# Kernel optimization log

Measured on AMD Instinct MI355X. Metric: run time of the kernel, lower is better.

## Reference

```python
import jax, jax.numpy as jnp
import numpy as np

B = 32
N_PER = 4096
N = B * N_PER
E = 2_097_152
D_IN = 32
D_OUT = 32
NUM_G_RELS = 14
NUM_ATTN_RELS = 10


def setup_inputs() -> dict:
    key = jax.random.key(0)
    ks = jax.random.split(key, 12)
    feat = jax.random.normal(ks[0], (N, D_IN), jnp.float32)
    src = jax.random.randint(ks[1], (E,), 0, N)
    dst = jax.random.randint(ks[2], (E,), 0, N)
    etype = jax.random.randint(ks[3], (E,), 0, NUM_ATTN_RELS)
    norm = jax.random.uniform(ks[4], (E,), jnp.float32)
    index1 = jax.random.randint(ks[5], (N,), 0, 2)  # path-node mask
    # first NUM_G_RELS nodes of each subgraph carry distinct relation slots -> unique scatter indices
    index2 = jnp.tile((jnp.arange(N_PER) < NUM_G_RELS).astype(jnp.int32), B)
    f2 = jnp.tile(jnp.arange(N_PER) % NUM_G_RELS, B).astype(jnp.int32)
    tar_rel = jnp.tile((jnp.arange(N_PER) == 0).astype(jnp.int32), B)  # one target node per graph
    s = 0.1
    W_w = jax.random.normal(ks[6], (D_IN, D_OUT), jnp.float32) * s
    b_w = jnp.zeros((D_OUT,), jnp.float32)
    W2 = jax.random.normal(ks[7], (3 * D_OUT, D_OUT), jnp.float32) * s
    b2 = jnp.zeros((D_OUT,), jnp.float32)
    attn_rel_emb = jax.random.normal(ks[8], (NUM_ATTN_RELS, D_OUT), jnp.float32) * s
    self_loop_w = jax.random.normal(ks[9], (D_IN, D_OUT), jnp.float32) * s
    W_line = jax.random.normal(ks[10], (D_OUT, D_OUT), jnp.float32) * s
    b_line = jnp.zeros((D_OUT,), jnp.float32)
    zero_path = jax.random.normal(ks[11], (1, D_OUT), jnp.float32) * s
    return {"feat": feat, "norm": norm, "W_w": W_w, "b_w": b_w, "W2": W2, "b2": b2,
            "attn_rel_emb": attn_rel_emb, "self_loop_w": self_loop_w, "W_line": W_line,
            "b_line": b_line, "zero_path": zero_path, "src": src, "dst": dst, "etype": etype,
            "index1": index1, "index2": index2, "f2": f2, "tar_rel": tar_rel,
            "n_per": N_PER, "num_g_rels": NUM_G_RELS}


def reference(feat, norm, W_w, b_w, W2, b2, attn_rel_emb, self_loop_w, W_line, b_line,
              zero_path, src, dst, etype, index1, index2, f2, tar_rel, n_per, num_g_rels):
    n_nodes, _ = feat.shape
    D = W_w.shape[1]
    # --- edge-wise relation-gated MLP (msg_func) ---
    et = attn_rel_emb[etype]                       # [E, D]
    w1 = feat[src] @ W_w + b_w                     # [E, D]
    cat = jnp.concatenate([et + w1, et - w1, et * w1], axis=1)  # [E, 3D]
    msg = (cat @ W2 + b2) * norm[:, None]          # [E, D] (edge weight w == 1)
    # --- SumAggregator: sum of msgs (alpha = ones) + self-loop term ---
    h = jax.ops.segment_sum(msg, dst, num_segments=n_nodes) + feat @ self_loop_w
    nf = jax.nn.relu(h @ W_line + b_line)          # cg_node_feats [N, D]
    # --- per-subgraph relation scatter + path attention (vectorized over batch) ---
    Bn = n_nodes // n_per
    nf_b = nf.reshape(Bn, n_per, D)
    mask2 = index2.reshape(Bn, n_per) != 0
    f2b = f2.reshape(Bn, n_per) + 1                # index_offset = 1
    write_idx = jnp.where(mask2, f2b, num_g_rels + 1)  # route masked rows to dump slot

    def scatter_one(idx, feats):
        buf = jnp.zeros((num_g_rels + 2, D), nf.dtype).at[idx].set(feats)
        return buf[:num_g_rels + 1]

    batch_rel_emds = jax.vmap(scatter_one)(write_idx, nf_b)  # [B, num_g_rels+1, D]
    tar1 = (tar_rel.reshape(Bn, n_per) == 1).astype(nf.dtype)
    target_rel_emd = jnp.einsum('bn,bnd->bd', tar1, nf_b)    # [B, D] (one-hot select)
    p1 = index1.reshape(Bn, n_per) == 1
    scores = jnp.where(p1, jnp.einsum('bnd,bd->bn', nf_b, target_rel_emd), -1e30)
    alpha = jax.nn.softmax(scores, axis=1)                   # segmented softmax over path nodes
    agg = jnp.einsum('bn,bnd->bd', alpha, nf_b)
    path_agg_emd = jnp.where(p1.any(axis=1)[:, None], agg, zero_path)  # [B, D]
    return batch_rel_emds, target_rel_emd, path_agg_emd
```

## Files before the change

kernel.cpp:

```cpp
#include <hip/hip_runtime.h>


#define N_PER_C 4096
#define NGR 14
#define NAR 10
#define NZB 68
#define KSP 8
#define BKN 128
#define NBMAX 1024
#define TSC 4096
#define CHK 2048

typedef unsigned short u16;
typedef unsigned int u32;
typedef _Float16 hv2 __attribute__((ext_vector_type(2)));
union U32H2 { u32 u; hv2 h; };

__device__ __forceinline__ float b2f(u16 u) {
    union { u32 i; float f; } x; x.i = ((u32)u) << 16; return x.f;
}
__device__ __forceinline__ u16 f2bf(float f) {
    union { float f; u32 i; } x; x.f = f;
    u32 r = x.i + 0x7fff + ((x.i >> 16) & 1);
    return (u16)(r >> 16);
}
__device__ __forceinline__ float LD(const void* p, size_t i, int isf32) {
    return isf32 ? ((const float*)p)[i] : b2f(((const u16*)p)[i]);
}
__device__ __forceinline__ void ST_OUT(void* p, size_t i, float v, int isf32) {
    if (isf32) ((float*)p)[i] = v;
    else ((u16*)p)[i] = f2bf(v);
}
__device__ __forceinline__ u32 pkh(float a, float b) {
    U32H2 c; c.h = (hv2){(_Float16)a, (_Float16)b}; return c.u;
}
__device__ __forceinline__ hv2 ash2(u32 w) { U32H2 c; c.u = w; return c.h; }

__device__ __forceinline__ int probe_flag(const u32* featw) {
    int cnt = 0;
#pragma unroll
    for (int i = 0; i < 256; i += 64) {
        u32 w = featw[i + (threadIdx.x & 63)];
        u32 lo = w & 0xffffu;
        u32 e = (lo >> 7) & 0xffu;
        cnt += ((e >= 100 && e <= 140) || lo == 0) ? 1 : 0;
    }
    unsigned long long m = __ballot(cnt >= 3);
    return (__popcll(m) < 32) ? 1 : 0;
}

__global__ __launch_bounds__(256) void k_prep(
        const u32* __restrict__ featw,
        const void* W_w, const void* b_w, const void* W2, const void* b2v,
        const void* attn, const void* slw, const void* W_line, const void* b_line,
        u32* __restrict__ outw, int out_size,
        float* Wwf, float* bwf, float* Af, float* slwf, float* Wlf, float* blf,
        float* Cf, float* ctf, u32* at2, u32* bcnt, int NB, int* flag) {
    int t = threadIdx.x;
    int b = blockIdx.x;
    int isf32 = probe_flag(featw);
    if (b < NZB) {
        int words = isf32 ? out_size : out_size / 2;
        for (int i = b * 256 + t; i < words; i += NZB * 256) outw[i] = 0;
        for (int i = b * 256 + t; i < NB; i += NZB * 256) bcnt[i] = 0u;
        return;
    }
    if (t == 0) flag[0] = isf32;
    for (int i = t; i < 1024; i += 256) {
        int k = i >> 5, c = i & 31;
        Wwf[i]  = LD(W_w, i, isf32);
        slwf[i] = LD(slw, i, isf32);
        Wlf[i]  = LD(W_line, i, isf32);
        Af[i]   = LD(W2, k * 32 + c, isf32) - LD(W2, (32 + k) * 32 + c, isf32);
        Cf[i]   = LD(W2, (64 + k) * 32 + c, isf32);
    }
    for (int i = t; i < NAR * 16; i += 256) {
        int tt = i >> 4, q = i & 15;
        at2[i] = pkh(LD(attn, tt * 32 + 2 * q, isf32),
                     LD(attn, tt * 32 + 2 * q + 1, isf32));
    }
    for (int i = t; i < NAR * 32; i += 256) {
        int tt = i >> 5, j = i & 31;
        float s = LD(b2v, j, isf32);
        for (int k = 0; k < 32; ++k) {
            float a = LD(attn, tt * 32 + k, isf32);
            s += a * (LD(W2, k * 32 + j, isf32) + LD(W2, (32 + k) * 32 + j, isf32));
        }
        ctf[i] = s;
    }
    if (t < 32) { bwf[t] = LD(b_w, t, isf32); blf[t] = LD(b_line, t, isf32); }
}

__global__ __launch_bounds__(256) void k1_node(const void* __restrict__ feat,
                        const float* __restrict__ Wwf,
                        const float* __restrict__ bwf, const float* __restrict__ slwf,
                        u32* __restrict__ gbuf, u32* __restrict__ h, int N,
                        const int* __restrict__ dst, u32* __restrict__ bcnt,
                        int E, int NB, const int* __restrict__ flag) {
    __shared__ u32 lh[NBMAX];
    int tid = threadIdx.x;
    int gid = blockIdx.x * 256 + tid;
    int isf32 = flag[0];
    for (int i = tid; i < NB; i += 256) lh[i] = 0u;
    __syncthreads();
    if (gid < N) {
        int n = gid;
        float f[32];
        if (isf32) {
            const float4* fr = (const float4*)((const float*)feat + (size_t)n * 32);
#pragma unroll
            for (int q = 0; q < 8; ++q) {
                float4 v = fr[q];
                f[q * 4 + 0] = v.x; f[q * 4 + 1] = v.y; f[q * 4 + 2] = v.z; f[q * 4 + 3] = v.w;
            }
        } else {
            const uint4* fr = (const uint4*)((const u16*)feat + (size_t)n * 32);
#pragma unroll
            for (int q = 0; q < 4; ++q) {
                uint4 v = fr[q];
                u32 ww[4] = {v.x, v.y, v.z, v.w};
#pragma unroll
                for (int r = 0; r < 4; ++r) {
                    f[q * 8 + 2 * r]     = b2f((u16)(ww[r] & 0xffff));
                    f[q * 8 + 2 * r + 1] = b2f((u16)(ww[r] >> 16));
                }
            }
        }
        float g[32], hh[32];
#pragma unroll
        for (int j = 0; j < 32; ++j) { g[j] = bwf[j]; hh[j] = 0.f; }
#pragma unroll
        for (int k = 0; k < 32; ++k) {
            float fk = f[k];
#pragma unroll
            for (int j = 0; j < 32; ++j) {
                g[j]  += fk * Wwf[k * 32 + j];
                hh[j] += fk * slwf[k * 32 + j];
            }
        }
        u32* go = gbuf + (size_t)n * 16;
#pragma unroll
        for (int q = 0; q < 16; ++q) go[q] = pkh(g[2 * q], g[2 * q + 1]);
        u32* ho = h + (size_t)n * 16;
#pragma unroll
        for (int q = 0; q < 16; ++q) ho[q] = pkh(hh[2 * q], hh[2 * q + 1]);
    }
    int EB = (E + gridDim.x - 1) / gridDim.x;
    int e0 = blockIdx.x * EB;
    int e1 = e0 + EB; if (e1 > E) e1 = E;
    for (int e = e0 + tid; e < e1; e += 256)
        atomicAdd(&lh[((u32)dst[e]) / BKN], 1u);
    __syncthreads();
    for (int i = tid; i < NB; i += 256) {
        u32 c = lh[i];
        if (c) atomicAdd(&bcnt[i], c);
    }
}

__global__ __launch_bounds__(256) void kB_scan(const u32* __restrict__ bcnt,
                                               u32* __restrict__ bbase,
                                               u32* __restrict__ bcur, int NB) {
    __shared__ u32 red[256];
    int tid = threadIdx.x;
    u32 c4[4]; u32 s = 0;
#pragma unroll
    for (int k = 0; k < 4; ++k) {
        int idx = tid * 4 + k;
        c4[k] = (idx < NB) ? bcnt[idx] : 0u;
        s += c4[k];
    }
    red[tid] = s;
    __syncthreads();
    for (int off = 1; off < 256; off <<= 1) {
        u32 v = (tid >= off) ? red[tid - off] : 0u;
        __syncthreads();
        red[tid] += v;
        __syncthreads();
    }
    u32 ex = red[tid] - s;
#pragma unroll
    for (int k = 0; k < 4; ++k) {
        int idx = tid * 4 + k;
        if (idx < NB) { bbase[idx] = ex; bcur[idx] = ex; ex += c4[k]; }
    }
    if (tid == 255) bbase[NB] = red[255];
}

__global__ __launch_bounds__(256) void kB_scatter(const int* __restrict__ src,
        const int* __restrict__ dst, const int* __restrict__ et,
        const void* __restrict__ norm, u32* __restrict__ bcur,
        uint2* __restrict__ pay, int E, int NB, const int* __restrict__ flag) {
    __shared__ u32 lcnt[NBMAX], loffA[NBMAX], loffB[NBMAX], lbase[NBMAX];
    __shared__ u32 red[256];
    __shared__ uint2 lbuf[TSC];
    __shared__ u16 lbkt[TSC];
    int tid = threadIdx.x;
    int base_e = blockIdx.x * TSC;
    int nval = E - base_e; if (nval > TSC) nval = TSC; if (nval < 0) nval = 0;
    int isf32 = flag[0];
    for (int i = tid; i < NB; i += 256) lcnt[i] = 0u;
    __syncthreads();
    u32 pk0[16], nw[16]; int bk[16];
#pragma unroll
    for (int i = 0; i < 16; ++i) {
        int e = base_e + i * 256 + tid;
        if (e < E) {
            int s = src[e], d = dst[e], t = et[e];
            float nr = LD(norm, e, isf32);
            pk0[i] = (u32)s | ((u32)t << 17) | ((u32)(d & (BKN - 1)) << 21);
            nw[i] = __float_as_uint(nr);
            bk[i] = ((u32)d) / BKN;
            atomicAdd(&lcnt[bk[i]], 1u);
        } else bk[i] = -1;
    }
    __syncthreads();
    u32 c4[4]; u32 s = 0;
#pragma unroll
    for (int k = 0; k < 4; ++k) {
        int idx = tid * 4 + k;
        c4[k] = (idx < NB) ? lcnt[idx] : 0u;
        s += c4[k];
    }
    red[tid] = s;
    __syncthreads();
    for (int off = 1; off < 256; off <<= 1) {
        u32 v = (tid >= off) ? red[tid - off] : 0u;
        __syncthreads();
        red[tid] += v;
        __syncthreads();
    }
    u32 ex = red[tid] - s;
#pragma unroll
    for (int k = 0; k < 4; ++k) {
        int idx = tid * 4 + k;
        if (idx < NB) { loffA[idx] = ex; loffB[idx] = ex; ex += c4[k]; }
    }
    __syncthreads();
    for (int b = tid; b < NB; b += 256) {
        u32 c = lcnt[b];
        if (c) lbase[b] = atomicAdd(&bcur[b], c);
    }
    __syncthreads();
#pragma unroll
    for (int i = 0; i < 16; ++i) {
        if (bk[i] >= 0) {
            u32 slot = atomicAdd(&loffB[bk[i]], 1u);
            lbuf[slot] = make_uint2(pk0[i], nw[i]);
            lbkt[slot] = (u16)bk[i];
        }
    }
    __syncthreads();
    for (int s2 = tid; s2 < nval; s2 += 256) {
        int b = lbkt[s2];
        u32 gpos = lbase[b] + (u32)s2 - loffA[b];
        pay[gpos] = lbuf[s2];
    }
}

__global__ __launch_bounds__(128) void kC_bucket(const u32* __restrict__ gbuf,
        const uint2* __restrict__ pay, const u32* __restrict__ bbase,
        const float* __restrict__ Af, const float* __restrict__ Cf,
        const float* __restrict__ ctf, const u32* __restrict__ at2,
        u32* __restrict__ h) {
    __shared__ uint2 lbuf[CHK];
    __shared__ u32 cnt_s[BKN];
    __shared__ u32 off_s[BKN];
    __shared__ u32 cur_s[BKN];
    __shared__ u32 scn_s[BKN];
    __shared__ u32 atl[16 * NAR];
    int tid = threadIdx.x;
    int b = blockIdx.x;
    for (int i = tid; i < 16 * NAR; i += 128) {
        int t = i >> 4, q = i & 15;
        atl[q * NAR + t] = at2[i];
    }
    int e0 = (int)bbase[b], e1 = (int)bbase[b + 1];

    float yg[32], x[32], nt[NAR];
#pragma unroll
    for (int j = 0; j < 32; ++j) { yg[j] = 0.f; x[j] = 0.f; }
#pragma unroll
    for (int t = 0; t < NAR; ++t) nt[t] = 0.f;

    for (int cb = e0; cb < e1; cb += CHK) {
        int nrec = e1 - cb; if (nrec > CHK) nrec = CHK;
        cnt_s[tid] = 0u;
        __syncthreads();
        for (int i = tid; i < nrec; i += 128)
            atomicAdd(&cnt_s[(pay[cb + i].x >> 21) & (BKN - 1)], 1u);
        __syncthreads();
        u32 myv = cnt_s[tid];
        scn_s[tid] = myv;
        __syncthreads();
        for (int s = 1; s < BKN; s <<= 1) {
            u32 v = (tid >= s) ? scn_s[tid - s] : 0u;
            __syncthreads();
            scn_s[tid] += v;
            __syncthreads();
        }
        u32 myoff = scn_s[tid] - myv;
        off_s[tid] = myoff;
        cur_s[tid] = myoff;
        __syncthreads();
        for (int i = tid; i < nrec; i += 128) {
            uint2 r = pay[cb + i];
            u32 d = (r.x >> 21) & (BKN - 1);
            u32 slot = atomicAdd(&cur_s[d], 1u);
            lbuf[slot] = r;
        }
        __syncthreads();
        {
            u32 myc = myv;
            uint2 rec = make_uint2(0u, 0u);
            uint4 GA = {0,0,0,0}, GB = {0,0,0,0}, GC = {0,0,0,0}, GD = {0,0,0,0};
            if (myc) {
                rec = lbuf[myoff];
                const uint4* g4 = (const uint4*)(gbuf + (size_t)(rec.x & 0x1FFFFu) * 16);
                GA = g4[0]; GB = g4[1]; GC = g4[2]; GD = g4[3];
            }
            for (u32 r = 0; r < myc; ++r) {
                uint2 rn = make_uint2(0u, 0u);
                uint4 HA = {0,0,0,0}, HB = {0,0,0,0}, HC = {0,0,0,0}, HD = {0,0,0,0};
                if (r + 1 < myc) {
                    rn = lbuf[myoff + r + 1];
                    const uint4* g4 = (const uint4*)(gbuf + (size_t)(rn.x & 0x1FFFFu) * 16);
                    HA = g4[0]; HB = g4[1]; HC = g4[2]; HD = g4[3];
                }
                int t = (int)((rec.x >> 17) & 0xFu);
                float nr = __uint_as_float(rec.y);
                u32 gw[16] = {GA.x, GA.y, GA.z, GA.w, GB.x, GB.y, GB.z, GB.w,
                              GC.x, GC.y, GC.z, GC.w, GD.x, GD.y, GD.z, GD.w};
#pragma unroll
                for (int q = 0; q < 16; ++q) {
                    hv2 gv = ash2(gw[q]);
                    hv2 av = ash2(atl[q * NAR + t]);
                    float ng0 = nr * (float)gv[0];
                    float ng1 = nr * (float)gv[1];
                    yg[2 * q]     += ng0;
                    yg[2 * q + 1] += ng1;
                    x[2 * q]      += ng0 * (float)av[0];
                    x[2 * q + 1]  += ng1 * (float)av[1];
                }
#pragma unroll
                for (int t2 = 0; t2 < NAR; ++t2) nt[t2] += (t2 == t) ? nr : 0.f;
                rec = rn;
                GA = HA; GB = HB; GC = HC; GD = HD;
            }
        }
        __syncthreads();
    }

    int n = b * BKN + tid;
    float o[32];
    const uint4* hr4 = (const uint4*)(h + (size_t)n * 16);
    uint4 v0 = hr4[0], v1 = hr4[1], v2 = hr4[2], v3 = hr4[3];
    u32 ww[16] = {v0.x, v0.y, v0.z, v0.w, v1.x, v1.y, v1.z, v1.w,
                  v2.x, v2.y, v2.z, v2.w, v3.x, v3.y, v3.z, v3.w};
#pragma unroll
    for (int r = 0; r < 16; ++r) {
        hv2 xh = ash2(ww[r]);
        o[2 * r]     = (float)xh[0];
        o[2 * r + 1] = (float)xh[1];
    }
#pragma unroll
    for (int t = 0; t < NAR; ++t) {
        float w = nt[t];
#pragma unroll
        for (int j = 0; j < 32; ++j) o[j] += w * ctf[t * 32 + j];
    }
#pragma unroll
    for (int k = 0; k < 32; ++k) {
        float a = yg[k], c = x[k];
#pragma unroll
        for (int j = 0; j < 32; ++j)
            o[j] += a * Af[k * 32 + j] + c * Cf[k * 32 + j];
    }
    u32* ho = h + (size_t)n * 16;
#pragma unroll
    for (int q = 0; q < 16; ++q) ho[q] = pkh(o[2 * q], o[2 * q + 1]);
}

__global__ __launch_bounds__(256) void k34_fused(const u32* __restrict__ h,
        const float* __restrict__ Wlf, const float* __restrict__ blf,
        const int* __restrict__ index2, const int* __restrict__ f2,
        const int* __restrict__ index1,
        void* __restrict__ out, size_t off_tar,
        float* __restrict__ part_m, float* __restrict__ part_l,
        float* __restrict__ part_a, const int* __restrict__ flag) {
    int blk = blockIdx.x;
    int b = blk / KSP, c = blk % KSP;
    int tid = threadIdx.x;
    int isf32 = flag[0];
    __shared__ float tg[32];
    __shared__ float red_m[256], red_l[256];
    __shared__ float red_a[256][33];

    if (tid < 32) {
        const u32* h0 = h + (size_t)b * N_PER_C * 16;
        float o = blf[tid];
#pragma unroll
        for (int k = 0; k < 32; ++k) {
            hv2 x = ash2(h0[k >> 1]);
            o += (float)x[k & 1] * Wlf[k * 32 + tid];
        }
        o = fmaxf(o, 0.f);
        tg[tid] = o;
        if (c == 0) ST_OUT(out, off_tar + (size_t)b * 32 + tid, o, isf32);
    }
    __syncthreads();
    float tv[32];
#pragma unroll
    for (int j = 0; j < 32; ++j) tv[j] = tg[j];

    float m = -1e30f, l = 0.f, a[32];
#pragma unroll
    for (int j = 0; j < 32; ++j) a[j] = 0.f;

    const int R = N_PER_C / KSP;
    for (int rr = 0; rr < R / 256; ++rr) {
        int n = b * N_PER_C + c * R + rr * 256 + tid;
        float hr[32];
        const uint4* h4 = (const uint4*)(h + (size_t)n * 16);
#pragma unroll
        for (int q = 0; q < 4; ++q) {
            uint4 v = h4[q];
            u32 ww[4] = {v.x, v.y, v.z, v.w};
#pragma unroll
            for (int r2 = 0; r2 < 4; ++r2) {
                hv2 x = ash2(ww[r2]);
                hr[q * 8 + 2 * r2]     = (float)x[0];
                hr[q * 8 + 2 * r2 + 1] = (float)x[1];
            }
        }
        float o[32];
#pragma unroll
        for (int j = 0; j < 32; ++j) o[j] = blf[j];
#pragma unroll
        for (int k = 0; k < 32; ++k) {
            float hk = hr[k];
#pragma unroll
            for (int j = 0; j < 32; ++j) o[j] += hk * Wlf[k * 32 + j];
        }
#pragma unroll
        for (int j = 0; j < 32; ++j) o[j] = fmaxf(o[j], 0.f);
        if (index2[n] != 0) {
            int idx = f2[n] + 1;
            if (idx >= 0 && idx <= NGR) {
                size_t bse = ((size_t)(b * (NGR + 1) + idx)) * 32;
#pragma unroll
                for (int j = 0; j < 32; ++j) ST_OUT(out, bse + j, o[j], isf32);
            }
        }
        if (index1[n] == 1) {
            float dot = 0.f;
#pragma unroll
            for (int j = 0; j < 32; ++j) dot += o[j] * tv[j];
            if (dot > m) {
                float cc = __expf(m - dot);
                l *= cc;
#pragma unroll
                for (int j = 0; j < 32; ++j) a[j] *= cc;
                m = dot;
            }
            float w = __expf(dot - m);
            l += w;
#pragma unroll
            for (int j = 0; j < 32; ++j) a[j] += w * o[j];
        }
    }
    red_m[tid] = m; red_l[tid] = l;
#pragma unroll
    for (int j = 0; j < 32; ++j) red_a[tid][j] = a[j];
    __syncthreads();
    for (int s = 128; s >= 1; s >>= 1) {
        if (tid < s) {
            float m1 = red_m[tid], m2 = red_m[tid + s];
            float M = fmaxf(m1, m2);
            float c1 = __expf(m1 - M), c2 = __expf(m2 - M);
            red_l[tid] = red_l[tid] * c1 + red_l[tid + s] * c2;
#pragma unroll
            for (int j = 0; j < 32; ++j)
                red_a[tid][j] = red_a[tid][j] * c1 + red_a[tid + s][j] * c2;
            red_m[tid] = M;
        }
        __syncthreads();
    }
    if (tid == 0) { part_m[blk] = red_m[0]; part_l[blk] = red_l[0]; }
    if (tid < 32) part_a[(size_t)blk * 32 + tid] = red_a[0][tid];
}

__global__ __launch_bounds__(64) void k4b_merge(const float* __restrict__ part_m,
                                                const float* __restrict__ part_l,
                                                const float* __restrict__ part_a,
                                                const void* __restrict__ zero_path,
                                                void* __restrict__ out,
                                                size_t off_path,
                                                const int* __restrict__ flag) {
    int b = blockIdx.x;
    int j = threadIdx.x;
    int isf32 = flag[0];
    if (j >= 32) return;
    float M = -1e30f;
#pragma unroll
    for (int i = 0; i < KSP; ++i) M = fmaxf(M, part_m[b * KSP + i]);
    float L = 0.f, A = 0.f;
#pragma unroll
    for (int i = 0; i < KSP; ++i) {
        float c = __expf(part_m[b * KSP + i] - M);
        L += part_l[b * KSP + i] * c;
        A += part_a[(size_t)(b * KSP + i) * 32 + j] * c;
    }
    float o = (L > 0.f) ? (A / L) : LD(zero_path, j, isf32);
    ST_OUT(out, off_path + (size_t)b * 32 + j, o, isf32);
}

extern "C" void kernel_launch(void* const* d_in, const int* in_sizes, int n_in,
                              void* d_out, int out_size, void* d_ws, size_t ws_size,
                              hipStream_t stream) {
    const void* feat     = d_in[0];
    const void* norm     = d_in[1];
    const void* W_w      = d_in[2];
    const void* b_w      = d_in[3];
    const void* W2       = d_in[4];
    const void* b2v      = d_in[5];
    const void* attn     = d_in[6];
    const void* slw      = d_in[7];
    const void* W_line   = d_in[8];
    const void* b_line   = d_in[9];
    const void* zeroPath = d_in[10];
    const int* src       = (const int*)d_in[11];
    const int* dst       = (const int*)d_in[12];
    const int* etype     = (const int*)d_in[13];
    const int* index1    = (const int*)d_in[14];
    const int* index2    = (const int*)d_in[15];
    const int* f2        = (const int*)d_in[16];

    int N  = in_sizes[0] / 32;
    int E  = in_sizes[1];
    int Bn = N / N_PER_C;
    int NB = N / BKN;

    char* base  = (char*)d_ws;
    int* flag   = (int*)base;
    float* Wwf  = (float*)(base + 64);
    float* bwf  = Wwf + 1024;
    float* Af   = bwf + 32;
    float* slwf = Af + 1024;
    float* Wlf  = slwf + 1024;
    float* blf  = Wlf + 1024;
    float* Cf   = blf + 32;
    float* ctf  = Cf + 1024;
    u32*  at2   = (u32*)(ctf + NAR * 32);
    float* part_m = (float*)(at2 + NAR * 16);
    float* part_l = part_m + (size_t)Bn * KSP;
    float* part_a = part_l + (size_t)Bn * KSP;
    char* pa = (char*)(part_a + (size_t)Bn * KSP * 32);
    pa = (char*)(((size_t)pa + 255) & ~(size_t)255);
    u32* bcnt  = (u32*)pa;
    u32* bbase = bcnt + NBMAX;
    u32* bcur  = bbase + NBMAX + 1;
    char* pb = (char*)(bcur + NBMAX);
    pb = (char*)(((size_t)pb + 255) & ~(size_t)255);
    uint2* pay  = (uint2*)pb;
    u32* gbuf   = (u32*)(pay + (size_t)E);
    u32* h      = gbuf + (size_t)N * 16;

    size_t off_tar  = (size_t)Bn * (NGR + 1) * 32;
    size_t off_path = off_tar + (size_t)Bn * 32;

    k_prep<<<NZB + 1, 256, 0, stream>>>((const u32*)feat,
                                        W_w, b_w, W2, b2v, attn, slw, W_line, b_line,
                                        (u32*)d_out, out_size,
                                        Wwf, bwf, Af, slwf, Wlf, blf,
                                        Cf, ctf, at2, bcnt, NB, flag);
    k1_node<<<(N + 255) / 256, 256, 0, stream>>>(feat, Wwf, bwf, slwf, gbuf, h, N,
                                                 dst, bcnt, E, NB, flag);
    kB_scan<<<1, 256, 0, stream>>>(bcnt, bbase, bcur, NB);
    kB_scatter<<<(E + TSC - 1) / TSC, 256, 0, stream>>>(src, dst, etype, norm,
                                                        bcur, pay, E, NB, flag);
    kC_bucket<<<NB, 128, 0, stream>>>(gbuf, pay, bbase, Af, Cf, ctf, at2, h);
    k34_fused<<<Bn * KSP, 256, 0, stream>>>(h, Wlf, blf, index2, f2, index1,
                                            d_out, off_tar,
                                            part_m, part_l, part_a, flag);
    k4b_merge<<<Bn, 64, 0, stream>>>(part_m, part_l, part_a, zeroPath,
                                     d_out, off_path, flag);
}
```

Before: 280.8 us.

## Split each destination node's edge accumulation across two threads in bucket kernel

The bucket aggregation kernel now runs 256 threads per block, with two lanes per destination node, each accumulating half of the 32 feature dimensions. The gather prefetch depth goes from one to two edges ahead, and the per-relation attention table is pre-converted to float2 in shared memory. The halves are combined with a lane shuffle, and only the even lane does the final projection and write. Chunk size also rises to 2560. This aims to raise memory-level parallelism and occupancy for the random gathers, at the cost of idle odd lanes in the epilogue and more shared memory.

```diff
diff --git a/kernel.cpp b/kernel.cpp
--- a/kernel.cpp
+++ b/kernel.cpp
@@ -9,7 +9,7 @@
 #define BKN 128
 #define NBMAX 1024
 #define TSC 4096
-#define CHK 2048
+#define CHK 2560
 
 typedef unsigned short u16;
 typedef unsigned int u32;
@@ -257,52 +257,54 @@
     }
 }
 
-__global__ __launch_bounds__(128) void kC_bucket(const u32* __restrict__ gbuf,
+__global__ __launch_bounds__(256) void kC_bucket(const u32* __restrict__ gbuf,
         const uint2* __restrict__ pay, const u32* __restrict__ bbase,
         const float* __restrict__ Af, const float* __restrict__ Cf,
         const float* __restrict__ ctf, const u32* __restrict__ at2,
         u32* __restrict__ h) {
     __shared__ uint2 lbuf[CHK];
-    __shared__ u32 cnt_s[BKN];
-    __shared__ u32 off_s[BKN];
-    __shared__ u32 cur_s[BKN];
-    __shared__ u32 scn_s[BKN];
-    __shared__ u32 atl[16 * NAR];
+    __shared__ u32 cnt_s[BKN], off_s[BKN], cur_s[BKN], scn_s[BKN];
+    __shared__ float2 atf[16 * NAR];
     int tid = threadIdx.x;
     int b = blockIdx.x;
-    for (int i = tid; i < 16 * NAR; i += 128) {
+    int lane = tid & 63;
+    int w = tid >> 6;
+    int nodeloc = w * 32 + (lane >> 1);
+    int hf = lane & 1;
+    int hbase = hf * 8;
+    for (int i = tid; i < 16 * NAR; i += 256) {
         int t = i >> 4, q = i & 15;
-        atl[q * NAR + t] = at2[i];
+        hv2 p = ash2(at2[i]);
+        atf[q * NAR + t] = make_float2((float)p[0], (float)p[1]);
     }
     int e0 = (int)bbase[b], e1 = (int)bbase[b + 1];
 
-    float yg[32], x[32], nt[NAR];
-#pragma unroll
-    for (int j = 0; j < 32; ++j) { yg[j] = 0.f; x[j] = 0.f; }
+    float yg[16], x[16], nt[NAR];
+#pragma unroll
+    for (int j = 0; j < 16; ++j) { yg[j] = 0.f; x[j] = 0.f; }
 #pragma unroll
     for (int t = 0; t < NAR; ++t) nt[t] = 0.f;
 
     for (int cb = e0; cb < e1; cb += CHK) {
         int nrec = e1 - cb; if (nrec > CHK) nrec = CHK;
-        cnt_s[tid] = 0u;
-        __syncthreads();
-        for (int i = tid; i < nrec; i += 128)
+        if (tid < BKN) cnt_s[tid] = 0u;
+        __syncthreads();
+        for (int i = tid; i < nrec; i += 256)
             atomicAdd(&cnt_s[(pay[cb + i].x >> 21) & (BKN - 1)], 1u);
         __syncthreads();
-        u32 myv = cnt_s[tid];
-        scn_s[tid] = myv;
+        u32 cv = 0;
+        if (tid < BKN) { cv = cnt_s[tid]; scn_s[tid] = cv; }
         __syncthreads();
         for (int s = 1; s < BKN; s <<= 1) {
-            u32 v = (tid >= s) ? scn_s[tid - s] : 0u;
+            u32 v = 0;
+            if (tid < BKN && tid >= s) v = scn_s[tid - s];
             __syncthreads();
-            scn_s[tid] += v;
+            if (tid < BKN) scn_s[tid] += v;
             __syncthreads();
         }
-        u32 myoff = scn_s[tid] - myv;
-        off_s[tid] = myoff;
-        cur_s[tid] = myoff;
-        __syncthreads();
-        for (int i = tid; i < nrec; i += 128) {
+        if (tid < BKN) { u32 o = scn_s[tid] - cv; off_s[tid] = o; cur_s[tid] = o; }
+        __syncthreads();
+        for (int i = tid; i < nrec; i += 256) {
             uint2 r = pay[cb + i];
             u32 d = (r.x >> 21) & (BKN - 1);
             u32 slot = atomicAdd(&cur_s[d], 1u);
@@ -310,74 +312,92 @@
         }
         __syncthreads();
         {
-            u32 myc = myv;
-            uint2 rec = make_uint2(0u, 0u);
-            uint4 GA = {0,0,0,0}, GB = {0,0,0,0}, GC = {0,0,0,0}, GD = {0,0,0,0};
-            if (myc) {
-                rec = lbuf[myoff];
-                const uint4* g4 = (const uint4*)(gbuf + (size_t)(rec.x & 0x1FFFFu) * 16);
-                GA = g4[0]; GB = g4[1]; GC = g4[2]; GD = g4[3];
+            u32 myc = cnt_s[nodeloc];
+            u32 myoff = off_s[nodeloc];
+            uint2 r0 = make_uint2(0u, 0u), r1 = make_uint2(0u, 0u);
+            uint4 A0 = make_uint4(0,0,0,0), B0 = make_uint4(0,0,0,0);
+            uint4 A1 = make_uint4(0,0,0,0), B1 = make_uint4(0,0,0,0);
+            if (myc > 0) {
+                r0 = lbuf[myoff];
+                const uint4* g4 = (const uint4*)(gbuf + (size_t)(r0.x & 0x1FFFFu) * 16 + hbase);
+                A0 = g4[0]; B0 = g4[1];
+            }
+            if (myc > 1) {
+                r1 = lbuf[myoff + 1];
+                const uint4* g4 = (const uint4*)(gbuf + (size_t)(r1.x & 0x1FFFFu) * 16 + hbase);
+                A1 = g4[0]; B1 = g4[1];
             }
             for (u32 r = 0; r < myc; ++r) {
                 uint2 rn = make_uint2(0u, 0u);
-                uint4 HA = {0,0,0,0}, HB = {0,0,0,0}, HC = {0,0,0,0}, HD = {0,0,0,0};
-                if (r + 1 < myc) {
-                    rn = lbuf[myoff + r + 1];
-                    const uint4* g4 = (const uint4*)(gbuf + (size_t)(rn.x & 0x1FFFFu) * 16);
-                    HA = g4[0]; HB = g4[1]; HC = g4[2]; HD = g4[3];
+                uint4 An = make_uint4(0,0,0,0), Bn = make_uint4(0,0,0,0);
+                if (r + 2 < myc) {
+                    rn = lbuf[myoff + r + 2];
+                    const uint4* g4 = (const uint4*)(gbuf + (size_t)(rn.x & 0x1FFFFu) * 16 + hbase);
+                    An = g4[0]; Bn = g4[1];
                 }
-                int t = (int)((rec.x >> 17) & 0xFu);
-                float nr = __uint_as_float(rec.y);
-                u32 gw[16] = {GA.x, GA.y, GA.z, GA.w, GB.x, GB.y, GB.z, GB.w,
-                              GC.x, GC.y, GC.z, GC.w, GD.x, GD.y, GD.z, GD.w};
-#pragma unroll
-                for (int q = 0; q < 16; ++q) {
+                int t = (int)((r0.x >> 17) & 0xFu);
+                float nr = __uint_as_float(r0.y);
+                u32 gw[8] = {A0.x, A0.y, A0.z, A0.w, B0.x, B0.y, B0.z, B0.w};
+#pragma unroll
+                for (int q = 0; q < 8; ++q) {
                     hv2 gv = ash2(gw[q]);
-                    hv2 av = ash2(atl[q * NAR + t]);
+                    float2 av = atf[(hbase + q) * NAR + t];
                     float ng0 = nr * (float)gv[0];
                     float ng1 = nr * (float)gv[1];
                     yg[2 * q]     += ng0;
                     yg[2 * q + 1] += ng1;
-                    x[2 * q]      += ng0 * (float)av[0];
-                    x[2 * q + 1]  += ng1 * (float)av[1];
+                    x[2 * q]      += ng0 * av.x;
+                    x[2 * q + 1]  += ng1 * av.y;
                 }
 #pragma unroll
                 for (int t2 = 0; t2 < NAR; ++t2) nt[t2] += (t2 == t) ? nr : 0.f;
-                rec = rn;
-                GA = HA; GB = HB; GC = HC; GD = HD;
-            }
-        }
-        __syncthreads();
-    }
-
-    int n = b * BKN + tid;
-    float o[32];
-    const uint4* hr4 = (const uint4*)(h + (size_t)n * 16);
-    uint4 v0 = hr4[0], v1 = hr4[1], v2 = hr4[2], v3 = hr4[3];
-    u32 ww[16] = {v0.x, v0.y, v0.z, v0.w, v1.x, v1.y, v1.z, v1.w,
-                  v2.x, v2.y, v2.z, v2.w, v3.x, v3.y, v3.z, v3.w};
-#pragma unroll
-    for (int r = 0; r < 16; ++r) {
-        hv2 xh = ash2(ww[r]);
-        o[2 * r]     = (float)xh[0];
-        o[2 * r + 1] = (float)xh[1];
-    }
-#pragma unroll
-    for (int t = 0; t < NAR; ++t) {
-        float w = nt[t];
-#pragma unroll
-        for (int j = 0; j < 32; ++j) o[j] += w * ctf[t * 32 + j];
-    }
-#pragma unroll
-    for (int k = 0; k < 32; ++k) {
-        float a = yg[k], c = x[k];
-#pragma unroll
-        for (int j = 0; j < 32; ++j)
-            o[j] += a * Af[k * 32 + j] + c * Cf[k * 32 + j];
-    }
-    u32* ho = h + (size_t)n * 16;
-#pragma unroll
-    for (int q = 0; q < 16; ++q) ho[q] = pkh(o[2 * q], o[2 * q + 1]);
+                r0 = r1; A0 = A1; B0 = B1;
+                r1 = rn; A1 = An; B1 = Bn;
+            }
+        }
+        __syncthreads();
+    }
+
+    float ygf[32], xf[32];
+#pragma unroll
+    for (int i = 0; i < 16; ++i) {
+        float oy = __shfl_xor(yg[i], 1);
+        float ox = __shfl_xor(x[i], 1);
+        ygf[i]      = hf ? oy    : yg[i];
+        ygf[16 + i] = hf ? yg[i] : oy;
+        xf[i]       = hf ? ox    : x[i];
+        xf[16 + i]  = hf ? x[i]  : ox;
+    }
+    if (hf == 0) {
+        int n = b * BKN + nodeloc;
+        float o[32];
+        const uint4* hr4 = (const uint4*)(h + (size_t)n * 16);
+        uint4 v0 = hr4[0], v1 = hr4[1], v2 = hr4[2], v3 = hr4[3];
+        u32 ww[16] = {v0.x, v0.y, v0.z, v0.w, v1.x, v1.y, v1.z, v1.w,
+                      v2.x, v2.y, v2.z, v2.w, v3.x, v3.y, v3.z, v3.w};
+#pragma unroll
+        for (int r = 0; r < 16; ++r) {
+            hv2 xh = ash2(ww[r]);
+            o[2 * r]     = (float)xh[0];
+            o[2 * r + 1] = (float)xh[1];
+        }
+#pragma unroll
+        for (int t = 0; t < NAR; ++t) {
+            float wv = nt[t];
+#pragma unroll
+            for (int j = 0; j < 32; ++j) o[j] += wv * ctf[t * 32 + j];
+        }
+#pragma unroll
+        for (int k = 0; k < 32; ++k) {
+            float a = ygf[k], c = xf[k];
+#pragma unroll
+            for (int j = 0; j < 32; ++j)
+                o[j] += a * Af[k * 32 + j] + c * Cf[k * 32 + j];
+        }
+        u32* ho = h + (size_t)n * 16;
+#pragma unroll
+        for (int q = 0; q < 16; ++q) ho[q] = pkh(o[2 * q], o[2 * q + 1]);
+    }
 }
 
 __global__ __launch_bounds__(256) void k34_fused(const u32* __restrict__ h,
@@ -578,7 +598,7 @@
     kB_scan<<<1, 256, 0, stream>>>(bcnt, bbase, bcur, NB);
     kB_scatter<<<(E + TSC - 1) / TSC, 256, 0, stream>>>(src, dst, etype, norm,
                                                         bcur, pay, E, NB, flag);
-    kC_bucket<<<NB, 128, 0, stream>>>(gbuf, pay, bbase, Af, Cf, ctf, at2, h);
+    kC_bucket<<<NB, 256, 0, stream>>>(gbuf, pay, bbase, Af, Cf, ctf, at2, h);
     k34_fused<<<Bn * KSP, 256, 0, stream>>>(h, Wlf, blf, index2, f2, index1,
                                             d_out, off_tar,
                                             part_m, part_l, part_a, flag);
```

Result: slower. 478.0 us (+70.2%).
